# Kernel tuning notes

Hardware: AMD Instinct MI355X
Metric: run time of the kernel (lower is better)

## Reference

```python
import jax, jax.numpy as jnp
import numpy as np

NUM_HEADS = 8
OUT_DIM = 16
IN_DIM = 128
N_NODES = 50000
N_EDGES = 1600000


def setup_inputs() -> dict:
    key = jax.random.key(0)
    ks = jax.random.split(key, 10)
    s = 1.0 / np.sqrt(IN_DIM)
    return {
        "h": jax.random.normal(ks[0], (N_NODES, IN_DIM), dtype=jnp.float32),
        "Qw": jax.random.normal(ks[1], (NUM_HEADS * OUT_DIM, IN_DIM), dtype=jnp.float32) * s,
        "Qb": jax.random.normal(ks[2], (NUM_HEADS * OUT_DIM,), dtype=jnp.float32) * 0.01,
        "Kw": jax.random.normal(ks[3], (NUM_HEADS * OUT_DIM, IN_DIM), dtype=jnp.float32) * s,
        "Kb": jax.random.normal(ks[4], (NUM_HEADS * OUT_DIM,), dtype=jnp.float32) * 0.01,
        "Vw": jax.random.normal(ks[5], (NUM_HEADS * OUT_DIM, IN_DIM), dtype=jnp.float32) * s,
        "Vb": jax.random.normal(ks[6], (NUM_HEADS * OUT_DIM,), dtype=jnp.float32) * 0.01,
        "src": jax.random.randint(ks[7], (N_EDGES,), 0, N_NODES, dtype=jnp.int64 if jax.config.jax_enable_x64 else jnp.int32).astype(jnp.int32),
        "dst": jax.random.randint(ks[8], (N_EDGES,), 0, N_NODES, dtype=jnp.int64 if jax.config.jax_enable_x64 else jnp.int32).astype(jnp.int32),
    }


def reference(h, Qw, Qb, Kw, Kb, Vw, Vb, src, dst):
    N = h.shape[0]
    H, D = NUM_HEADS, OUT_DIM
    # Q/K/V projections (torch Linear: x @ W.T + b), viewed as [N, H, D]
    Q = (h @ Qw.T + Qb).reshape(N, H, D)
    K = (h @ Kw.T + Kb).reshape(N, H, D)
    V = (h @ Vw.T + Vb).reshape(N, H, D)

    # dgl.add_self_loop: append (i, i) edges for every node
    loop = jnp.arange(N, dtype=src.dtype)
    s = jnp.concatenate([src, loop])
    d = jnp.concatenate([dst, loop])

    # src_dot_dst quirk: matmul(K_src [H,D], Q_dst^T [D,H]).sum(-1)
    # => score[e, h] = K_src[e, h] . (sum over heads of Q_dst[e])
    Qsum = Q.sum(axis=1)  # [N, D]
    score = jnp.einsum("ehd,ed->eh", K[s], Qsum[d])  # [E', H]
    score = jnp.exp(jnp.clip(score / np.float32(np.sqrt(D)), -5.0, 5.0))

    # scatter-sum of weighted V and scores to destination nodes
    wV = jax.ops.segment_sum(V[s] * score[:, :, None], d, num_segments=N)  # [N, H, D]
    z = jax.ops.segment_sum(score, d, num_segments=N)  # [N, H]

    head_out = wV / z[:, :, None]  # self-loops guarantee z > 0
    return head_out.mean(axis=1)  # [N, D]
```

## Files before the change

kernel.cpp:

```cpp
#include <hip/hip_runtime.h>
#include <hip/hip_fp16.h>
#include <math.h>

#define NNODES 50000
#define IND    128
#define NH     8
#define OD     16
#define NEDGE  1600000
#define NOUT   272
#define NBUCK  391
#define BCAP   4608
#define SCAP   56
#define P1B    196
#define PB2    782

typedef _Float16 half8 __attribute__((ext_vector_type(8)));
typedef _Float16 h2t   __attribute__((ext_vector_type(2)));
typedef float    floatx4 __attribute__((ext_vector_type(4)));

static __device__ __forceinline__ h2t u2h(unsigned int u) {
    union { unsigned int u; h2t h; } x; x.u = u; return x.h;
}
static __device__ __forceinline__ float qdot(uint4 k, uint4 q, float p) {
    p = __builtin_amdgcn_fdot2(u2h(k.x), u2h(q.x), p, false);
    p = __builtin_amdgcn_fdot2(u2h(k.y), u2h(q.y), p, false);
    p = __builtin_amdgcn_fdot2(u2h(k.z), u2h(q.z), p, false);
    p = __builtin_amdgcn_fdot2(u2h(k.w), u2h(q.w), p, false);
    return p;
}
static __device__ __forceinline__ void vacc8(uint4 vA, uint4 vB, h2t sc2, float* acc) {
    unsigned lo, hi;
    lo = __builtin_amdgcn_perm(vB.x, vA.x, 0x05040100u);
    hi = __builtin_amdgcn_perm(vB.x, vA.x, 0x07060302u);
    acc[0] = __builtin_amdgcn_fdot2(u2h(lo), sc2, acc[0], false);
    acc[1] = __builtin_amdgcn_fdot2(u2h(hi), sc2, acc[1], false);
    lo = __builtin_amdgcn_perm(vB.y, vA.y, 0x05040100u);
    hi = __builtin_amdgcn_perm(vB.y, vA.y, 0x07060302u);
    acc[2] = __builtin_amdgcn_fdot2(u2h(lo), sc2, acc[2], false);
    acc[3] = __builtin_amdgcn_fdot2(u2h(hi), sc2, acc[3], false);
    lo = __builtin_amdgcn_perm(vB.z, vA.z, 0x05040100u);
    hi = __builtin_amdgcn_perm(vB.z, vA.z, 0x07060302u);
    acc[4] = __builtin_amdgcn_fdot2(u2h(lo), sc2, acc[4], false);
    acc[5] = __builtin_amdgcn_fdot2(u2h(hi), sc2, acc[5], false);
    lo = __builtin_amdgcn_perm(vB.w, vA.w, 0x05040100u);
    hi = __builtin_amdgcn_perm(vB.w, vA.w, 0x07060302u);
    acc[6] = __builtin_amdgcn_fdot2(u2h(lo), sc2, acc[6], false);
    acc[7] = __builtin_amdgcn_fdot2(u2h(hi), sc2, acc[7], false);
}

__global__ __launch_bounds__(256) void k1_scatter_w16(
    const int* __restrict__ src, const int* __restrict__ dst,
    unsigned int* __restrict__ ebuck, unsigned short* __restrict__ counts,
    const float* __restrict__ Qw, const float* __restrict__ Qb,
    const float* __restrict__ Kw, const float* __restrict__ Kb,
    const float* __restrict__ Vw, const float* __restrict__ Vb,
    _Float16* __restrict__ W16s, float* __restrict__ b_all)
{
    const int t = threadIdx.x;

    if (blockIdx.x < P1B) {
        __shared__ int bcnt[NBUCK];
        for (int i = t; i < NBUCK; i += 256) bcnt[i] = 0;
        __syncthreads();

        const int blk = blockIdx.x;
        const int e0  = blk * 8192;
        const int nq  = (min(8192, NEDGE - e0)) >> 2;
        const int4* s4 = (const int4*)(src + e0);
        const int4* d4 = (const int4*)(dst + e0);

        uint4 ev4[8];
        unsigned int rkp[16];
#pragma unroll
        for (int j = 0; j < 8; j++) {
            int qi = j * 256 + t;
            if (qi < nq) {
                int4 ss = s4[qi];
                int4 dd = d4[qi];
                unsigned int v0 = (((unsigned)dd.x >> 7) << 23) | ((unsigned)ss.x << 7) | ((unsigned)dd.x & 127u);
                unsigned int v1 = (((unsigned)dd.y >> 7) << 23) | ((unsigned)ss.y << 7) | ((unsigned)dd.y & 127u);
                unsigned int v2 = (((unsigned)dd.z >> 7) << 23) | ((unsigned)ss.z << 7) | ((unsigned)dd.z & 127u);
                unsigned int v3 = (((unsigned)dd.w >> 7) << 23) | ((unsigned)ss.w << 7) | ((unsigned)dd.w & 127u);
                ev4[j] = make_uint4(v0, v1, v2, v3);
                unsigned r0 = atomicAdd(&bcnt[v0 >> 23], 1);
                unsigned r1 = atomicAdd(&bcnt[v1 >> 23], 1);
                unsigned r2 = atomicAdd(&bcnt[v2 >> 23], 1);
                unsigned r3 = atomicAdd(&bcnt[v3 >> 23], 1);
                rkp[2 * j]     = r0 | (r1 << 16);
                rkp[2 * j + 1] = r2 | (r3 << 16);
            }
        }
        __syncthreads();
#pragma unroll
        for (int j = 0; j < 8; j++) {
            int qi = j * 256 + t;
            if (qi < nq) {
                uint4 v = ev4[j];
                unsigned p0 = rkp[2 * j], p1 = rkp[2 * j + 1];
                unsigned r0 = p0 & 0xFFFFu, r1 = p0 >> 16;
                unsigned r2 = p1 & 0xFFFFu, r3 = p1 >> 16;
                if (r0 < SCAP) ebuck[((size_t)(v.x >> 23) * P1B + blk) * SCAP + r0] = v.x;
                if (r1 < SCAP) ebuck[((size_t)(v.y >> 23) * P1B + blk) * SCAP + r1] = v.y;
                if (r2 < SCAP) ebuck[((size_t)(v.z >> 23) * P1B + blk) * SCAP + r2] = v.z;
                if (r3 < SCAP) ebuck[((size_t)(v.w >> 23) * P1B + blk) * SCAP + r3] = v.w;
            }
        }
        __syncthreads();
        for (int i = t; i < NBUCK; i += 256)
            counts[(size_t)blk * NBUCK + i] = (unsigned short)min(bcnt[i], SCAP);
        return;
    }

    for (int i = t; i < NOUT * IND; i += 256) {
        int r = i >> 7, c = i & 127;
        float v;
        if (r < 128)       v = Kw[r * IND + c];
        else if (r < 256)  v = Vw[(r - 128) * IND + c];
        else {
            v = 0.f;
#pragma unroll
            for (int hh = 0; hh < NH; hh++) v += Qw[((hh << 4) + (r - 256)) * IND + c];
        }
        int ti = r >> 4, cl = r & 15, ks = c >> 5, quad = (c >> 3) & 3, e = c & 7;
        W16s[((((ti << 2) + ks) << 6) + quad * 16 + cl) * 8 + e] = (_Float16)v;
    }
    for (int i = t; i < NOUT; i += 256) {
        float v;
        if (i < 128)      v = Kb[i];
        else if (i < 256) v = Vb[i - 128];
        else {
            v = 0.f;
#pragma unroll
            for (int hh = 0; hh < NH; hh++) v += Qb[(hh << 4) + (i - 256)];
        }
        b_all[i] = v;
    }
}

__global__ __launch_bounds__(256) void k2_proj_group(
    const float* __restrict__ hmat,
    const _Float16* __restrict__ W16s, const float* __restrict__ b_all,
    __half* __restrict__ KVbuf, _Float16* __restrict__ Qs16,
    const unsigned int* __restrict__ ebuck, const unsigned short* __restrict__ counts,
    int* __restrict__ offs, int* __restrict__ count,
    unsigned short* __restrict__ eidx16)
{
    const int t = threadIdx.x;

    if (blockIdx.x < PB2) {
        const int wave = t >> 6;
        const int l    = t & 63;
        const int cl   = l & 15;
        const int quad = l >> 4;
        const int m0   = blockIdx.x * 64 + wave * 16;

        const int arow = min(m0 + cl, NNODES - 1);
        const float* ab = hmat + (size_t)arow * IND + quad * 8;
        half8 afrag[4];
#pragma unroll
        for (int ks = 0; ks < 4; ks++) {
            float4 x = *(const float4*)(ab + ks * 32);
            float4 y = *(const float4*)(ab + ks * 32 + 4);
            half8 o;
            o[0] = (_Float16)x.x; o[1] = (_Float16)x.y;
            o[2] = (_Float16)x.z; o[3] = (_Float16)x.w;
            o[4] = (_Float16)y.x; o[5] = (_Float16)y.y;
            o[6] = (_Float16)y.z; o[7] = (_Float16)y.w;
            afrag[ks] = o;
        }

        const int rowbase = m0 + quad * 4;
        const half8* Wf = (const half8*)W16s;

#pragma unroll 4
        for (int ti = 0; ti < 17; ti++) {
            floatx4 acc = {0.f, 0.f, 0.f, 0.f};
#pragma unroll
            for (int ks = 0; ks < 4; ks++)
                acc = __builtin_amdgcn_mfma_f32_16x16x32_f16(
                    afrag[ks], Wf[(((ti << 2) + ks) << 6) + l], acc, 0, 0, 0);

            const float bias = b_all[ti * 16 + cl];
            if (ti < 16) {
                const int col = ti * 16 + cl;
#pragma unroll
                for (int r = 0; r < 4; r++) {
                    int node = rowbase + r;
                    if (node < NNODES)
                        KVbuf[(size_t)node * 256 + col] = __float2half_rn(acc[r] + bias);
                }
            } else {
#pragma unroll
                for (int r = 0; r < 4; r++) {
                    int node = rowbase + r;
                    if (node < NNODES)
                        Qs16[(size_t)node * OD + cl] = (_Float16)(acc[r] + bias);
                }
            }
        }
        return;
    }

    __shared__ int esh[BCAP];
    __shared__ int csh[256];
    __shared__ int cbase[256];
    __shared__ int sdc[256];
    __shared__ int cnt[128];
    __shared__ int sdn[128];
    __shared__ int base128[128];

    const int b = blockIdx.x - PB2;

    csh[t] = (t < P1B) ? (int)counts[(size_t)t * NBUCK + b] : 0;
    __syncthreads();
    sdc[t] = csh[t];
    __syncthreads();
    for (int ofs = 1; ofs < 256; ofs <<= 1) {
        int x = (t >= ofs) ? sdc[t - ofs] : 0;
        __syncthreads();
        sdc[t] += x;
        __syncthreads();
    }
    cbase[t] = sdc[t] - csh[t];
    __syncthreads();
    const int Eb = sdc[P1B - 1];

    const unsigned int* cells = ebuck + (size_t)b * P1B * SCAP;
    for (int idx = t; idx < P1B * SCAP; idx += 256) {
        int j = idx / SCAP;
        int r = idx - j * SCAP;
        if (r < csh[j]) {
            int p = cbase[j] + r;
            if (p < BCAP) esh[p] = (int)cells[idx];
        }
    }
    if (t < 128) cnt[t] = 0;
    __syncthreads();

    int rk[18];
#pragma unroll
    for (int j = 0; j < 18; j++) {
        int i = j * 256 + t;
        if (i < Eb) rk[j] = atomicAdd(&cnt[esh[i] & 127], 1);
    }
    __syncthreads();

    if (t < 128) sdn[t] = cnt[t];
    __syncthreads();
    for (int ofs = 1; ofs < 128; ofs <<= 1) {
        int x = 0;
        if (t < 128 && t >= ofs) x = sdn[t - ofs];
        __syncthreads();
        if (t < 128) sdn[t] += x;
        __syncthreads();
    }
    if (t < 128) {
        int excl = sdn[t] - cnt[t];
        base128[t] = excl;
        int node = (b << 7) + t;
        if (node < NNODES) { offs[node] = b * BCAP + excl; count[node] = cnt[t]; }
    }
    __syncthreads();

#pragma unroll
    for (int j = 0; j < 18; j++) {
        int i = j * 256 + t;
        if (i < Eb) {
            int v = esh[i];
            eidx16[(size_t)b * BCAP + base128[v & 127] + rk[j]] =
                (unsigned short)((v >> 7) & 0xFFFFu);
        }
    }
}

__global__ __launch_bounds__(256) void k3_gather(
    const uint4* __restrict__ KV4, const uint4* __restrict__ Qs16u4,
    const int* __restrict__ offs, const int* __restrict__ count,
    const unsigned short* __restrict__ eidx16,
    float* __restrict__ out)
{
    const int n = blockIdx.x * 4 + (threadIdx.x >> 6);
    const int l = threadIdx.x & 63;
    if (n >= NNODES) return;

    const int lh = l & 15;
    const int eg = l >> 4;
    const int la = 2 * eg, lb = 2 * eg + 1;

    const uint4 qh = Qs16u4[n * 2 + (lh & 1)];

    const int off   = offs[n];
    const int total = count[n] + 1;

    float acc[8] = {0.f, 0.f, 0.f, 0.f, 0.f, 0.f, 0.f, 0.f};
    float zacc = 0.f;

    for (int base = 0; base < total; base += 64) {
        const int gi = base + l;
        int id = n;
        if (gi > 0) id = (gi < total) ? (int)eidx16[off + gi - 1] : 0;
        const int steps = min(64, total - base);

        int sA = __shfl(id, la, 64), sB = __shfl(id, lb, 64);
        uint4 kA0 = KV4[(size_t)sA * 32 + lh];
        uint4 vA0 = KV4[(size_t)sA * 32 + 16 + lh];
        uint4 kB0 = KV4[(size_t)sB * 32 + lh];
        uint4 vB0 = KV4[(size_t)sB * 32 + 16 + lh];
        int n1a = 8 + la, n1b = 8 + lb;
        int sA1 = __shfl(id, (n1a < 64) ? n1a : 0, 64);
        int sB1 = __shfl(id, (n1b < 64) ? n1b : 0, 64);
        uint4 kA1 = KV4[(size_t)sA1 * 32 + lh];
        uint4 vA1 = KV4[(size_t)sA1 * 32 + 16 + lh];
        uint4 kB1 = KV4[(size_t)sB1 * 32 + lh];
        uint4 vB1 = KV4[(size_t)sB1 * 32 + 16 + lh];

        for (int j = 0; j < steps; j += 8) {
            uint4 kA2, vA2, kB2, vB2;
            if (j + 16 < steps) {
                int n2a = j + 16 + la, n2b = j + 16 + lb;
                int sA2 = __shfl(id, (n2a < 64) ? n2a : 0, 64);
                int sB2 = __shfl(id, (n2b < 64) ? n2b : 0, 64);
                kA2 = KV4[(size_t)sA2 * 32 + lh];
                vA2 = KV4[(size_t)sA2 * 32 + 16 + lh];
                kB2 = KV4[(size_t)sB2 * 32 + lh];
                vB2 = KV4[(size_t)sB2 * 32 + 16 + lh];
            }
            float pA = qdot(kA0, qh, 0.f);
            float pB = qdot(kB0, qh, 0.f);
            pA += __shfl_xor(pA, 1, 64);
            pB += __shfl_xor(pB, 1, 64);
            float scA = __expf(fminf(5.f, fmaxf(-5.f, pA * 0.25f)));
            float scB = __expf(fminf(5.f, fmaxf(-5.f, pB * 0.25f)));
            if (j + la >= steps) scA = 0.f;
            if (j + lb >= steps) scB = 0.f;
            zacc += scA + scB;
            h2t sc2; sc2.x = (_Float16)scA; sc2.y = (_Float16)scB;
            vacc8(vA0, vB0, sc2, acc);
            kA0 = kA1; vA0 = vA1; kB0 = kB1; vB0 = vB1;
            kA1 = kA2; vA1 = vA2; kB1 = kB2; vB1 = vB2;
        }
    }

#pragma unroll
    for (int i = 0; i < 8; i++) {
        acc[i] += __shfl_xor(acc[i], 16, 64);
        acc[i] += __shfl_xor(acc[i], 32, 64);
    }
    zacc += __shfl_xor(zacc, 16, 64);
    zacc += __shfl_xor(zacc, 32, 64);

    const float inv = 1.f / zacc;
    float r[8];
#pragma unroll
    for (int i = 0; i < 8; i++) r[i] = acc[i] * inv;
#pragma unroll
    for (int i = 0; i < 8; i++) {
        r[i] += __shfl_xor(r[i], 2, 64);
        r[i] += __shfl_xor(r[i], 4, 64);
        r[i] += __shfl_xor(r[i], 8, 64);
    }
    if (l < 2) {
        float4* op = (float4*)(out + (size_t)n * OD + l * 8);
        op[0] = make_float4(r[0] * 0.125f, r[1] * 0.125f, r[2] * 0.125f, r[3] * 0.125f);
        op[1] = make_float4(r[4] * 0.125f, r[5] * 0.125f, r[6] * 0.125f, r[7] * 0.125f);
    }
}

extern "C" void kernel_launch(void* const* d_in, const int* in_sizes, int n_in,
                              void* d_out, int out_size, void* d_ws, size_t ws_size,
                              hipStream_t stream)
{
    const float* h  = (const float*)d_in[0];
    const float* Qw = (const float*)d_in[1];
    const float* Qb = (const float*)d_in[2];
    const float* Kw = (const float*)d_in[3];
    const float* Kb = (const float*)d_in[4];
    const float* Vw = (const float*)d_in[5];
    const float* Vb = (const float*)d_in[6];
    const int*   src = (const int*)d_in[7];
    const int*   dst = (const int*)d_in[8];

    char* ws = (char*)d_ws;
    _Float16* W16s  = (_Float16*)ws;                   ws += (size_t)NOUT * IND * 2;
    float*    b_all = (float*)ws;                      ws += 288 * 4;
    __half*   KVbuf = (__half*)ws;                     ws += (size_t)NNODES * 256 * 2;
    _Float16* Qs16  = (_Float16*)ws;                   ws += (size_t)NNODES * OD * 2;
    int*      offs   = (int*)ws;                       ws += (size_t)NNODES * 4;
    int*      count  = (int*)ws;                       ws += (size_t)NNODES * 4;
    unsigned short* counts = (unsigned short*)ws;      ws += (size_t)P1B * NBUCK * 2 + 64;
    unsigned int*   ebuck  = (unsigned int*)ws;        ws += (size_t)NBUCK * P1B * SCAP * 4;
    unsigned short* eidx16 = (unsigned short*)ws;      ws += (size_t)NBUCK * BCAP * 2;

    k1_scatter_w16<<<P1B + 1, 256, 0, stream>>>(
        src, dst, ebuck, counts, Qw, Qb, Kw, Kb, Vw, Vb, W16s, b_all);

    k2_proj_group<<<PB2 + NBUCK, 256, 0, stream>>>(
        h, W16s, b_all, KVbuf, Qs16, ebuck, counts, offs, count, eidx16);

    k3_gather<<<(NNODES + 3) / 4, 256, 0, stream>>>(
        (const uint4*)KVbuf, (const uint4*)Qs16, offs, count, eidx16, (float*)d_out);
}
```

Before: 259.6 us.

## Split K/V into per-head tables and gather per head with a combine pass

Stores K and V as head-major tables (head, node, dim) and launches the gather kernel per (head, node group), so each block touches only one head's 32-byte K/V rows. The idea is that the gathered working set per pass becomes a single head's table, which should fit in cache better than the full interleaved 512-byte rows. Per-head results go to an fp16 intermediate, and a new combine kernel averages them. In exchange, the edge-index list and offsets are read eight times, the software prefetch pipeline is removed, an extra launch and intermediate buffer are added, and per-head outputs are rounded to fp16.

```diff
diff --git a/kernel.cpp b/kernel.cpp
--- a/kernel.cpp
+++ b/kernel.cpp
@@ -21,31 +21,9 @@
 static __device__ __forceinline__ h2t u2h(unsigned int u) {
     union { unsigned int u; h2t h; } x; x.u = u; return x.h;
 }
-static __device__ __forceinline__ float qdot(uint4 k, uint4 q, float p) {
-    p = __builtin_amdgcn_fdot2(u2h(k.x), u2h(q.x), p, false);
-    p = __builtin_amdgcn_fdot2(u2h(k.y), u2h(q.y), p, false);
-    p = __builtin_amdgcn_fdot2(u2h(k.z), u2h(q.z), p, false);
-    p = __builtin_amdgcn_fdot2(u2h(k.w), u2h(q.w), p, false);
-    return p;
-}
-static __device__ __forceinline__ void vacc8(uint4 vA, uint4 vB, h2t sc2, float* acc) {
-    unsigned lo, hi;
-    lo = __builtin_amdgcn_perm(vB.x, vA.x, 0x05040100u);
-    hi = __builtin_amdgcn_perm(vB.x, vA.x, 0x07060302u);
-    acc[0] = __builtin_amdgcn_fdot2(u2h(lo), sc2, acc[0], false);
-    acc[1] = __builtin_amdgcn_fdot2(u2h(hi), sc2, acc[1], false);
-    lo = __builtin_amdgcn_perm(vB.y, vA.y, 0x05040100u);
-    hi = __builtin_amdgcn_perm(vB.y, vA.y, 0x07060302u);
-    acc[2] = __builtin_amdgcn_fdot2(u2h(lo), sc2, acc[2], false);
-    acc[3] = __builtin_amdgcn_fdot2(u2h(hi), sc2, acc[3], false);
-    lo = __builtin_amdgcn_perm(vB.z, vA.z, 0x05040100u);
-    hi = __builtin_amdgcn_perm(vB.z, vA.z, 0x07060302u);
-    acc[4] = __builtin_amdgcn_fdot2(u2h(lo), sc2, acc[4], false);
-    acc[5] = __builtin_amdgcn_fdot2(u2h(hi), sc2, acc[5], false);
-    lo = __builtin_amdgcn_perm(vB.w, vA.w, 0x05040100u);
-    hi = __builtin_amdgcn_perm(vB.w, vA.w, 0x07060302u);
-    acc[6] = __builtin_amdgcn_fdot2(u2h(lo), sc2, acc[6], false);
-    acc[7] = __builtin_amdgcn_fdot2(u2h(hi), sc2, acc[7], false);
+static __device__ __forceinline__ float2 u2f2(unsigned int u) {
+    union { unsigned int u; __half2 h; } x; x.u = u;
+    return __half22float2(x.h);
 }
 
 __global__ __launch_bounds__(256) void k1_scatter_w16(
@@ -140,7 +118,8 @@
 __global__ __launch_bounds__(256) void k2_proj_group(
     const float* __restrict__ hmat,
     const _Float16* __restrict__ W16s, const float* __restrict__ b_all,
-    __half* __restrict__ KVbuf, _Float16* __restrict__ Qs16,
+    _Float16* __restrict__ Ktab, _Float16* __restrict__ Vtab,
+    _Float16* __restrict__ Qs16,
     const unsigned int* __restrict__ ebuck, const unsigned short* __restrict__ counts,
     int* __restrict__ offs, int* __restrict__ count,
     unsigned short* __restrict__ eidx16)
@@ -181,13 +160,21 @@
                     afrag[ks], Wf[(((ti << 2) + ks) << 6) + l], acc, 0, 0, 0);
 
             const float bias = b_all[ti * 16 + cl];
-            if (ti < 16) {
-                const int col = ti * 16 + cl;
+            if (ti < 8) {
 #pragma unroll
                 for (int r = 0; r < 4; r++) {
                     int node = rowbase + r;
                     if (node < NNODES)
-                        KVbuf[(size_t)node * 256 + col] = __float2half_rn(acc[r] + bias);
+                        Ktab[((size_t)ti * NNODES + node) * OD + cl] =
+                            (_Float16)(acc[r] + bias);
+                }
+            } else if (ti < 16) {
+#pragma unroll
+                for (int r = 0; r < 4; r++) {
+                    int node = rowbase + r;
+                    if (node < NNODES)
+                        Vtab[((size_t)(ti - 8) * NNODES + node) * OD + cl] =
+                            (_Float16)(acc[r] + bias);
                 }
             } else {
 #pragma unroll
@@ -274,96 +261,91 @@
 }
 
 __global__ __launch_bounds__(256) void k3_gather(
-    const uint4* __restrict__ KV4, const uint4* __restrict__ Qs16u4,
+    const _Float16* __restrict__ Ktab, const _Float16* __restrict__ Vtab,
+    const _Float16* __restrict__ Qs16,
     const int* __restrict__ offs, const int* __restrict__ count,
     const unsigned short* __restrict__ eidx16,
-    float* __restrict__ out)
-{
-    const int n = blockIdx.x * 4 + (threadIdx.x >> 6);
-    const int l = threadIdx.x & 63;
-    if (n >= NNODES) return;
-
-    const int lh = l & 15;
-    const int eg = l >> 4;
-    const int la = 2 * eg, lb = 2 * eg + 1;
-
-    const uint4 qh = Qs16u4[n * 2 + (lh & 1)];
+    _Float16* __restrict__ hout)
+{
+    const int h  = blockIdx.x & 7;
+    const int n  = (blockIdx.x >> 3) * 4 + (threadIdx.x >> 6);
+    const int l  = threadIdx.x & 63;
+    const int g  = l >> 2;
+    const int j4 = l & 3;
+
+    const _Float16* Kh = Ktab + (size_t)h * NNODES * OD;
+    const _Float16* Vh = Vtab + (size_t)h * NNODES * OD;
+
+    const uint2 qv = *(const uint2*)(Qs16 + (size_t)n * OD + j4 * 4);
 
     const int off   = offs[n];
     const int total = count[n] + 1;
 
-    float acc[8] = {0.f, 0.f, 0.f, 0.f, 0.f, 0.f, 0.f, 0.f};
-    float zacc = 0.f;
+    float a0 = 0.f, a1 = 0.f, a2 = 0.f, a3 = 0.f, z = 0.f;
 
     for (int base = 0; base < total; base += 64) {
         const int gi = base + l;
         int id = n;
-        if (gi > 0) id = (gi < total) ? (int)eidx16[off + gi - 1] : 0;
+        if (gi > 0 && gi < total)
+            id = (int)__builtin_nontemporal_load(eidx16 + off + gi - 1);
         const int steps = min(64, total - base);
 
-        int sA = __shfl(id, la, 64), sB = __shfl(id, lb, 64);
-        uint4 kA0 = KV4[(size_t)sA * 32 + lh];
-        uint4 vA0 = KV4[(size_t)sA * 32 + 16 + lh];
-        uint4 kB0 = KV4[(size_t)sB * 32 + lh];
-        uint4 vB0 = KV4[(size_t)sB * 32 + 16 + lh];
-        int n1a = 8 + la, n1b = 8 + lb;
-        int sA1 = __shfl(id, (n1a < 64) ? n1a : 0, 64);
-        int sB1 = __shfl(id, (n1b < 64) ? n1b : 0, 64);
-        uint4 kA1 = KV4[(size_t)sA1 * 32 + lh];
-        uint4 vA1 = KV4[(size_t)sA1 * 32 + 16 + lh];
-        uint4 kB1 = KV4[(size_t)sB1 * 32 + lh];
-        uint4 vB1 = KV4[(size_t)sB1 * 32 + 16 + lh];
-
-        for (int j = 0; j < steps; j += 8) {
-            uint4 kA2, vA2, kB2, vB2;
-            if (j + 16 < steps) {
-                int n2a = j + 16 + la, n2b = j + 16 + lb;
-                int sA2 = __shfl(id, (n2a < 64) ? n2a : 0, 64);
-                int sB2 = __shfl(id, (n2b < 64) ? n2b : 0, 64);
-                kA2 = KV4[(size_t)sA2 * 32 + lh];
-                vA2 = KV4[(size_t)sA2 * 32 + 16 + lh];
-                kB2 = KV4[(size_t)sB2 * 32 + lh];
-                vB2 = KV4[(size_t)sB2 * 32 + 16 + lh];
-            }
-            float pA = qdot(kA0, qh, 0.f);
-            float pB = qdot(kB0, qh, 0.f);
-            pA += __shfl_xor(pA, 1, 64);
-            pB += __shfl_xor(pB, 1, 64);
-            float scA = __expf(fminf(5.f, fmaxf(-5.f, pA * 0.25f)));
-            float scB = __expf(fminf(5.f, fmaxf(-5.f, pB * 0.25f)));
-            if (j + la >= steps) scA = 0.f;
-            if (j + lb >= steps) scB = 0.f;
-            zacc += scA + scB;
-            h2t sc2; sc2.x = (_Float16)scA; sc2.y = (_Float16)scB;
-            vacc8(vA0, vB0, sc2, acc);
-            kA0 = kA1; vA0 = vA1; kB0 = kB1; vB0 = vB1;
-            kA1 = kA2; vA1 = vA2; kB1 = kB2; vB1 = vB2;
-        }
-    }
-
-#pragma unroll
-    for (int i = 0; i < 8; i++) {
-        acc[i] += __shfl_xor(acc[i], 16, 64);
-        acc[i] += __shfl_xor(acc[i], 32, 64);
-    }
-    zacc += __shfl_xor(zacc, 16, 64);
-    zacc += __shfl_xor(zacc, 32, 64);
-
-    const float inv = 1.f / zacc;
-    float r[8];
-#pragma unroll
-    for (int i = 0; i < 8; i++) r[i] = acc[i] * inv;
-#pragma unroll
-    for (int i = 0; i < 8; i++) {
-        r[i] += __shfl_xor(r[i], 2, 64);
-        r[i] += __shfl_xor(r[i], 4, 64);
-        r[i] += __shfl_xor(r[i], 8, 64);
-    }
-    if (l < 2) {
-        float4* op = (float4*)(out + (size_t)n * OD + l * 8);
-        op[0] = make_float4(r[0] * 0.125f, r[1] * 0.125f, r[2] * 0.125f, r[3] * 0.125f);
-        op[1] = make_float4(r[4] * 0.125f, r[5] * 0.125f, r[6] * 0.125f, r[7] * 0.125f);
-    }
+        for (int r = 0; r < steps; r += 16) {
+            const int e = r + g;
+            const int sid = __shfl(id, e, 64);
+            const uint2 kk = *(const uint2*)(Kh + (size_t)sid * OD + j4 * 4);
+            const uint2 vv = *(const uint2*)(Vh + (size_t)sid * OD + j4 * 4);
+
+            float p = __builtin_amdgcn_fdot2(u2h(kk.y), u2h(qv.y),
+                      __builtin_amdgcn_fdot2(u2h(kk.x), u2h(qv.x), 0.f, false), false);
+            p += __shfl_xor(p, 1, 64);
+            p += __shfl_xor(p, 2, 64);
+            float sc = __expf(fminf(5.f, fmaxf(-5.f, p * 0.25f)));
+            if (e >= steps) sc = 0.f;
+            z += sc;
+            float2 f0 = u2f2(vv.x);
+            float2 f1 = u2f2(vv.y);
+            a0 = fmaf(f0.x, sc, a0); a1 = fmaf(f0.y, sc, a1);
+            a2 = fmaf(f1.x, sc, a2); a3 = fmaf(f1.y, sc, a3);
+        }
+    }
+
+#pragma unroll
+    for (int m = 4; m <= 32; m <<= 1) {
+        a0 += __shfl_xor(a0, m, 64);
+        a1 += __shfl_xor(a1, m, 64);
+        a2 += __shfl_xor(a2, m, 64);
+        a3 += __shfl_xor(a3, m, 64);
+        z  += __shfl_xor(z,  m, 64);
+    }
+
+    if (l < 4) {
+        const float inv = 1.f / z;
+        h2t p0, p1;
+        p0.x = (_Float16)(a0 * inv); p0.y = (_Float16)(a1 * inv);
+        p1.x = (_Float16)(a2 * inv); p1.y = (_Float16)(a3 * inv);
+        union { struct { h2t a, b; } h; unsigned long long u; } pk;
+        pk.h.a = p0; pk.h.b = p1;
+        __builtin_nontemporal_store(pk.u,
+            (unsigned long long*)(hout + ((size_t)h * NNODES + n) * OD + l * 4));
+    }
+}
+
+__global__ __launch_bounds__(256) void k4_combine(
+    const _Float16* __restrict__ hout, float* __restrict__ out)
+{
+    const int t = blockIdx.x * 256 + threadIdx.x;
+    if (t >= NNODES * 4) return;
+    const int n = t >> 2, q = t & 3;
+    float sx = 0.f, sy = 0.f, sz = 0.f, sw = 0.f;
+#pragma unroll
+    for (int h = 0; h < NH; h++) {
+        uint2 u = *(const uint2*)(hout + ((size_t)h * NNODES + n) * OD + q * 4);
+        float2 f0 = u2f2(u.x);
+        float2 f1 = u2f2(u.y);
+        sx += f0.x; sy += f0.y; sz += f1.x; sw += f1.y;
+    }
+    ((float4*)out)[t] = make_float4(sx * 0.125f, sy * 0.125f, sz * 0.125f, sw * 0.125f);
 }
 
 extern "C" void kernel_launch(void* const* d_in, const int* in_sizes, int n_in,
@@ -383,8 +365,10 @@
     char* ws = (char*)d_ws;
     _Float16* W16s  = (_Float16*)ws;                   ws += (size_t)NOUT * IND * 2;
     float*    b_all = (float*)ws;                      ws += 288 * 4;
-    __half*   KVbuf = (__half*)ws;                     ws += (size_t)NNODES * 256 * 2;
+    _Float16* Ktab  = (_Float16*)ws;                   ws += (size_t)NH * NNODES * OD * 2;
+    _Float16* Vtab  = (_Float16*)ws;                   ws += (size_t)NH * NNODES * OD * 2;
     _Float16* Qs16  = (_Float16*)ws;                   ws += (size_t)NNODES * OD * 2;
+    _Float16* hout  = (_Float16*)ws;                   ws += (size_t)NH * NNODES * OD * 2;
     int*      offs   = (int*)ws;                       ws += (size_t)NNODES * 4;
     int*      count  = (int*)ws;                       ws += (size_t)NNODES * 4;
     unsigned short* counts = (unsigned short*)ws;      ws += (size_t)P1B * NBUCK * 2 + 64;
@@ -395,8 +379,10 @@
         src, dst, ebuck, counts, Qw, Qb, Kw, Kb, Vw, Vb, W16s, b_all);
 
     k2_proj_group<<<PB2 + NBUCK, 256, 0, stream>>>(
-        h, W16s, b_all, KVbuf, Qs16, ebuck, counts, offs, count, eidx16);
-
-    k3_gather<<<(NNODES + 3) / 4, 256, 0, stream>>>(
-        (const uint4*)KVbuf, (const uint4*)Qs16, offs, count, eidx16, (float*)d_out);
-}
+        h, W16s, b_all, Ktab, Vtab, Qs16, ebuck, counts, offs, count, eidx16);
+
+    k3_gather<<<(NNODES / 4) * NH, 256, 0, stream>>>(
+        Ktab, Vtab, Qs16, offs, count, eidx16, hout);
+
+    k4_combine<<<(NNODES * 4 + 255) / 256, 256, 0, stream>>>(hout, (float*)d_out);
+}
```

New measurement: 335.9 us. 29.4% more time.
